# Kernel optimization log

Measured on AMD Instinct MI355X. Metric: run time of the kernel, lower is better.

## Reference

```python
import jax, jax.numpy as jnp
import numpy as np

B, L = 2048, 64          # sentence pairs, leaves per balanced binary tree
V, IN, M, HID, NC = 50000, 300, 150, 50, 5


def setup_inputs() -> dict:
    key = jax.random.key(0)
    ks = jax.random.split(key, 16)
    lin = lambda k, fi, fo: jax.random.normal(k, (fi, fo), jnp.float32) / np.sqrt(fi).astype(np.float32)
    bias = lambda k, fo: jax.random.normal(k, (fo,), jnp.float32) * 0.01
    return {
        "ltokens": jax.random.randint(ks[0], (B, L), 0, V, dtype=jnp.int32),
        "rtokens": jax.random.randint(ks[1], (B, L), 0, V, dtype=jnp.int32),
        "emb":   jax.random.normal(ks[2], (V, IN), jnp.float32),
        "Wioux": lin(ks[3], IN, 3 * M), "bioux": bias(ks[4], 3 * M),
        "Wiouh": lin(ks[5], M, 3 * M), "biouh": bias(ks[6], 3 * M),
        "Wfx":   lin(ks[7], IN, M),    "bfx":   bias(ks[8], M),
        "Wfh":   lin(ks[9], M, M),     "bfh":   bias(ks[10], M),
        "Wh":    lin(ks[11], 2 * M, HID), "bh": bias(ks[12], HID),
        "Wp":    lin(ks[13], HID, NC),    "bp": bias(ks[14], NC),
    }


def _split_iou(iou, m):
    return iou[..., :m], iou[..., m:2 * m], iou[..., 2 * m:]


def _encode(tokens, emb, Wioux, bioux, Wiouh, biouh, Wfh, bfh):
    m = Wfh.shape[0]
    x = emb[tokens]                                   # [B, L, IN]
    # Leaves: child_h = child_c = 0, so iouh contributes only its bias and fc = 0.
    iou = x @ Wioux + bioux + biouh                   # [B, L, 3M]
    i, o, u = _split_iou(iou, m)
    c = jax.nn.sigmoid(i) * jnp.tanh(u)
    h = jax.nn.sigmoid(o) * jnp.tanh(c)
    # Internal nodes level by level (inputs=None branch of node_forward).
    while h.shape[1] > 1:
        Bq, n, _ = h.shape
        ch = h.reshape(Bq, n // 2, 2, m)              # children h
        cc = c.reshape(Bq, n // 2, 2, m)              # children c
        iou = ch.sum(axis=2) @ Wiouh + biouh          # child-sum
        i, o, u = _split_iou(iou, m)
        f = jax.nn.sigmoid(ch @ Wfh + bfh)            # per-child forget gate
        c = jax.nn.sigmoid(i) * jnp.tanh(u) + (f * cc).sum(axis=2)
        h = jax.nn.sigmoid(o) * jnp.tanh(c)
    # ROOT in the original just passes its single child's state through.
    return h[:, 0]                                    # [B, M]


def reference(ltokens, rtokens, emb, Wioux, bioux, Wiouh, biouh, Wfx, bfx, Wfh, bfh, Wh, bh, Wp, bp):
    lh = _encode(ltokens, emb, Wioux, bioux, Wiouh, biouh, Wfh, bfh)
    rh = _encode(rtokens, emb, Wioux, bioux, Wiouh, biouh, Wfh, bfh)
    vec = jnp.concatenate([lh * rh, jnp.abs(lh - rh)], axis=-1)   # [B, 2M]
    mid = jax.nn.sigmoid(vec @ Wh + bh)
    return jax.nn.log_softmax(mid @ Wp + bp, axis=-1)             # [B, NC]
```

## Files before the change

### kernel.cpp

```cpp
#include <hip/hip_runtime.h>
#include <hip/hip_bf16.h>
#include <math.h>

constexpr int B_   = 2048;
constexpr int L_   = 64;
constexpr int V_   = 50000;
constexpr int IN_  = 300;
constexpr int M_   = 150;
constexpr int HID_ = 50;
constexpr int NC_  = 5;

constexpr int KP_  = 160;
constexpr int CS_  = 152;
constexpr int GN_  = 608;
constexpr int GNT_ = 19;
constexpr int GKC_ = 5;
constexpr int GCH_ = GN_ * 32;
constexpr int GQS_ = GN_ * 8;
constexpr int LEAF_N  = 480;
constexpr int LEAF_NT = 15;
constexpr int LEAF_KC = 10;
constexpr int LEAF_CH = LEAF_N * 32;
constexpr int LEAF_QS = LEAF_N * 8;

typedef float f32x4  __attribute__((ext_vector_type(4)));
typedef short bf16x8 __attribute__((ext_vector_type(8)));
typedef short short4v __attribute__((ext_vector_type(4)));

__device__ __forceinline__ float rcp_f(float x) { return __builtin_amdgcn_rcpf(x); }
__device__ __forceinline__ float sgm(float x)   { return rcp_f(1.0f + __expf(-x)); }
__device__ __forceinline__ float tanh_f(float x){ return 1.0f - 2.0f * rcp_f(1.0f + __expf(2.0f * x)); }

__device__ __forceinline__ short f2bs(float f) {
    union { __hip_bfloat16 h; short s; } u; u.h = __float2bfloat16(f); return u.s;
}
__device__ __forceinline__ float bs2f(short s) {
    union { short s; __hip_bfloat16 h; } u; u.s = s; return __bfloat162float(u.h);
}

__device__ __forceinline__ void gl_lds16(const short* g, short* l) {
    __builtin_amdgcn_global_load_lds(
        (const __attribute__((address_space(1))) unsigned int*)g,
        (__attribute__((address_space(3))) unsigned int*)l, 16, 0, 0);
}

__global__ __launch_bounds__(256) void prep_kernel(
    const float* __restrict__ Wioux, const float* __restrict__ Wiouh,
    const float* __restrict__ Wfh, short* __restrict__ Bg, short* __restrict__ Bx)
{
    const int tid = blockIdx.x * blockDim.x + threadIdx.x;
    const int nthr = gridDim.x * blockDim.x;
    const int tot1 = GKC_ * GCH_;
    for (int idx = tid; idx < tot1; idx += nthr) {
        const int kc = idx / GCH_;
        int rem = idx % GCH_;
        const int q = rem / GQS_; rem %= GQS_;
        const int n = rem / 8, j = rem % 8;
        const int k = kc * 32 + q * 8 + j;
        const int m = n >> 2, g = n & 3;
        float v = 0.0f;
        if (k < M_ && m < M_)
            v = (g < 3) ? Wiouh[k * 450 + g * 150 + m] : Wfh[k * M_ + m];
        Bg[idx] = f2bs(v);
    }
    const int tot2 = LEAF_KC * LEAF_CH;
    for (int idx = tid; idx < tot2; idx += nthr) {
        const int kc = idx / LEAF_CH;
        int rem = idx % LEAF_CH;
        const int q = rem / LEAF_QS; rem %= LEAF_QS;
        const int n = rem / 8, j = rem % 8;
        const int k = kc * 32 + q * 8 + j;
        float v = (k < IN_ && n < 450) ? Wioux[k * 450 + n] : 0.0f;
        Bx[idx] = f2bs(v);
    }
}

__global__ __launch_bounds__(512) void leafE_gemm(
    const float* __restrict__ emb, const short* __restrict__ Bx,
    const short* __restrict__ Bg,
    const float* __restrict__ bioux, const float* __restrict__ biouh,
    const float* __restrict__ bfh, short* __restrict__ LeafE)
{
    __shared__ __align__(16) char smem[81248];
    short* Bs     = (short*)smem;
    short* AsF    = (short*)(smem + 38912);
    short* As     = AsF;
    short* CinS   = (short*)(smem + 59392);
    float* bias_s = (float*)(smem + 78848);
    float* Es     = (float*)smem;
    short* Os     = Bs;

    const int t = threadIdx.x;
    const int v0 = blockIdx.x * 64;
    const int w = t >> 6, lane = t & 63;
    const int mt = w & 3;
    const int lr = lane & 15, quad = lane >> 4;

    if (t < 600) bias_s[t] = (t < 450) ? (bioux[t] + biouh[t]) : bfh[t - 450];

    const int nt1 = (w >> 2) * LEAF_NT;
    f32x4 acc[GNT_];
    #pragma unroll
    for (int i = 0; i < LEAF_NT; i++) { acc[i][0] = 0; acc[i][1] = 0; acc[i][2] = 0; acc[i][3] = 0; }

    const int arow = t >> 3, apart = t & 7;
    const int av = v0 + arow;
    const int aq = apart >> 1, aj = (apart & 1) * 4;

    for (int kc = 0; kc < LEAF_KC; kc++) {
        const short* bsrc = Bx + (size_t)kc * LEAF_CH;
        #pragma unroll
        for (int i = 0; i < 3; i++)
            gl_lds16(bsrc + (i * 512 + t) * 8, Bs + (i * 512 + (t & ~63)) * 8);
        if (t < 384)
            gl_lds16(bsrc + (1536 + t) * 8, Bs + (1536 + (t & ~63)) * 8);
        {
            const int k0 = kc * 32 + apart * 4;
            float4 x = make_float4(0.f, 0.f, 0.f, 0.f);
            if (av < V_ && k0 < IN_) x = *(const float4*)&emb[(size_t)av * IN_ + k0];
            short4v s;
            s[0] = f2bs(x.x); s[1] = f2bs(x.y); s[2] = f2bs(x.z); s[3] = f2bs(x.w);
            *(short4v*)&As[aq * 512 + arow * 8 + aj] = s;
        }
        __syncthreads();
        bf16x8 a = *(const bf16x8*)&As[quad * 512 + (mt * 16 + lr) * 8];
        #pragma unroll
        for (int i = 0; i < LEAF_NT; i++) {
            bf16x8 b = *(const bf16x8*)&Bs[quad * LEAF_QS + ((nt1 + i) * 16 + lr) * 8];
            acc[i] = __builtin_amdgcn_mfma_f32_16x16x32_bf16(a, b, acc[i], 0, 0, 0);
        }
        __syncthreads();
    }

    for (int mc = 0; mc < 4; mc++) {
        if (mt == mc) {
            #pragma unroll
            for (int i = 0; i < LEAF_NT; i++) {
                const int col = (nt1 + i) * 16 + lr;
                #pragma unroll
                for (int r = 0; r < 4; r++) Es[(quad * 4 + r) * LEAF_N + col] = acc[i][r];
            }
        }
        __syncthreads();
        for (int p = t; p < 640; p += 512) {
            const int rl = p / 40, Q = p % 40;
            const int m0 = 4 * Q;
            short4v hq = {0, 0, 0, 0}, cq = {0, 0, 0, 0};
            if (Q < 38) {
                #pragma unroll
                for (int jj = 0; jj < 4; jj++) {
                    const int m = m0 + jj;
                    if (m < M_) {
                        const float i_ = Es[rl * LEAF_N + m]       + bias_s[m];
                        const float o_ = Es[rl * LEAF_N + m + 150] + bias_s[m + 150];
                        const float u_ = Es[rl * LEAF_N + m + 300] + bias_s[m + 300];
                        const float c = sgm(i_) * tanh_f(u_);
                        const float h = sgm(o_) * tanh_f(c);
                        hq[jj] = f2bs(h); cq[jj] = f2bs(c);
                    }
                }
            }
            const int row = mc * 16 + rl;
            const int kc = m0 >> 5, q = (m0 >> 3) & 3, j0 = m0 & 7;
            *(short4v*)&AsF[(kc * 4 + q) * 512 + row * 8 + j0] = hq;
            if (m0 < M_) *(short4v*)&CinS[row * CS_ + m0] = cq;
        }
        __syncthreads();
    }

    const int nt2 = (w >> 2) * GNT_;
    #pragma unroll
    for (int i = 0; i < GNT_; i++) { acc[i][0] = 0; acc[i][1] = 0; acc[i][2] = 0; acc[i][3] = 0; }

    for (int kc = 0; kc < GKC_; kc++) {
        const short* bsrc = Bg + (size_t)kc * GCH_;
        #pragma unroll
        for (int i = 0; i < 4; i++)
            gl_lds16(bsrc + (i * 512 + t) * 8, Bs + (i * 512 + (t & ~63)) * 8);
        if (t < 384)
            gl_lds16(bsrc + (2048 + t) * 8, Bs + (2048 + (t & ~63)) * 8);
        __syncthreads();
        bf16x8 a = *(const bf16x8*)&AsF[kc * 2048 + quad * 512 + (mt * 16 + lr) * 8];
        #pragma unroll
        for (int i = 0; i < GNT_; i++) {
            bf16x8 b = *(const bf16x8*)&Bs[quad * GQS_ + ((nt2 + i) * 16 + lr) * 8];
            acc[i] = __builtin_amdgcn_mfma_f32_16x16x32_bf16(a, b, acc[i], 0, 0, 0);
        }
        __syncthreads();
    }

    const int c = lane & 15;
    for (int ph = 0; ph < 2; ph++) {
        if ((mt >> 1) == ph) {
            const int rbase = 16 * (mt & 1) + 4 * quad;
            #pragma unroll
            for (int i = 0; i < GNT_; i++) {
                const int col = (nt2 + i) * 16 + c;
                const int m = col >> 2, g = col & 3;
                #pragma unroll
                for (int r = 0; r < 4; r++) {
                    short ov;
                    if (g == 3) {
                        if (m < M_) {
                            const float cc = bs2f(CinS[(32 * ph + rbase + r) * CS_ + m]);
                            ov = f2bs(sgm(acc[i][r] + bias_s[450 + m]) * cc);
                        } else ov = 0;
                    } else ov = f2bs(acc[i][r]);
                    Os[(rbase + r) * GN_ + col] = ov;
                }
            }
        }
        __syncthreads();
        const int vb = v0 + 32 * ph;
        const int4* os4 = (const int4*)Os;
        for (int u = t; u < 2432; u += 512) {
            const int row = u / 76;
            if (vb + row < V_)
                ((int4*)(LeafE + (size_t)(vb + row) * GN_))[u - row * 76] = os4[u];
        }
        __syncthreads();
    }
}

__device__ __forceinline__ void level_epilogue(
    const f32x4* acc, int mt, int nt0, int lane,
    const short* CinS, int cstride, const float* bias_s, short* Hs, short* Cs)
{
    const int q = lane >> 4, c = lane & 15, g = c & 3, lb = lane & ~3;
    #pragma unroll
    for (int i = 0; i < GNT_; i++) {
        const int col = (nt0 + i) * 16 + c;
        const int m = col >> 2;
        const float vA = acc[i][0] + acc[i][1];
        const float vB = acc[i][2] + acc[i][3];
        const float iA = __shfl(vA, lb), oA = __shfl(vA, lb + 1), uA = __shfl(vA, lb + 2);
        const float iB = __shfl(vB, lb), oB = __shfl(vB, lb + 1), uB = __shfl(vB, lb + 2);
        const float fA0 = __shfl(acc[i][0], lb + 3), fA1 = __shfl(acc[i][1], lb + 3);
        const float fB0 = __shfl(acc[i][2], lb + 3), fB1 = __shfl(acc[i][3], lb + 3);
        if (g < 2 && m < M_) {
            const float iv = g ? iB : iA, ov = g ? oB : oA, uv = g ? uB : uA;
            const float fl = g ? fB0 : fA0, fr = g ? fB1 : fA1;
            const int node = 8 * mt + 2 * q + g;
            const int ch = 16 * mt + 4 * q + 2 * g;
            const float cl = bs2f(CinS[ch * cstride + m]);
            const float cr = bs2f(CinS[(ch + 1) * cstride + m]);
            const float bf = bias_s[450 + m];
            const float cv = sgm(iv + bias_s[m]) * tanh_f(uv + bias_s[m + 300])
                           + sgm(fl + bf) * cl + sgm(fr + bf) * cr;
            const float hv = sgm(ov + bias_s[m + 150]) * tanh_f(cv);
            Hs[node * KP_ + m] = f2bs(hv);
            Cs[node * KP_ + m] = f2bs(cv);
        }
    }
}

__global__ __launch_bounds__(512) void level1_fused(
    const int* __restrict__ ltok, const int* __restrict__ rtok,
    const short* __restrict__ LeafE, const short* __restrict__ Bg,
    const float* __restrict__ biouh, const float* __restrict__ bfh,
    short* __restrict__ Hout, short* __restrict__ Cout)
{
    __shared__ __align__(16) char smem[81248];
    short* Bs     = (short*)smem;
    short* AsF    = (short*)(smem + 38912);
    short* CinS   = (short*)(smem + 59392);
    float* bias_s = (float*)(smem + 78848);
    short* Hs = Bs;
    short* Cs = Bs + 32 * KP_;

    const int t = threadIdx.x;
    const int out0 = blockIdx.x * 32;
    const int w = t >> 6, lane = t & 63;
    const int mt = w & 3, nt0 = (w >> 2) * GNT_;
    const int lr = lane & 15, quad = lane >> 4;

    {
        const short* bsrc = Bg;
        #pragma unroll
        for (int i = 0; i < 4; i++)
            gl_lds16(bsrc + (i * 512 + t) * 8, Bs + (i * 512 + (t & ~63)) * 8);
        if (t < 384)
            gl_lds16(bsrc + (2048 + t) * 8, Bs + (2048 + (t & ~63)) * 8);
    }
    if (t < 600) bias_s[t] = (t < 450) ? biouh[t] : bfh[t - 450];
    __syncthreads();

    {
        const int row = t >> 3, qs = t & 7;
        const int half = B_ * L_;
        const int gidx = blockIdx.x * 128 + 2 * row;
        const int tl = (gidx < half) ? ltok[gidx] : rtok[gidx - half];
        const int tr = (gidx + 1 < half) ? ltok[gidx + 1] : rtok[gidx + 1 - half];
        const short* el = LeafE + (size_t)tl * GN_;
        const short* er = LeafE + (size_t)tr * GN_;
        #pragma unroll
        for (int s = 0; s < 5; s++) {
            const int Q = qs + 8 * s;
            short4v hq = {0, 0, 0, 0}, cq = {0, 0, 0, 0};
            if (Q < 38) {
                union { int4 v[2]; short s16[16]; } ue, ur;
                ue.v[0] = *(const int4*)(el + Q * 16);
                ue.v[1] = *(const int4*)(el + Q * 16 + 8);
                ur.v[0] = *(const int4*)(er + Q * 16);
                ur.v[1] = *(const int4*)(er + Q * 16 + 8);
                #pragma unroll
                for (int jj = 0; jj < 4; jj++) {
                    const int m = 4 * Q + jj;
                    if (m < M_) {
                        const float i_ = bs2f(ue.s16[4 * jj])     + bs2f(ur.s16[4 * jj])     + bias_s[m];
                        const float o_ = bs2f(ue.s16[4 * jj + 1]) + bs2f(ur.s16[4 * jj + 1]) + bias_s[m + 150];
                        const float u_ = bs2f(ue.s16[4 * jj + 2]) + bs2f(ur.s16[4 * jj + 2]) + bias_s[m + 300];
                        const float fc = bs2f(ue.s16[4 * jj + 3]) + bs2f(ur.s16[4 * jj + 3]);
                        const float cv = sgm(i_) * tanh_f(u_) + fc;
                        const float hv = sgm(o_) * tanh_f(cv);
                        hq[jj] = f2bs(hv); cq[jj] = f2bs(cv);
                    }
                }
            }
            const int m0 = 4 * Q;
            const int kc = m0 >> 5, q = (m0 >> 3) & 3, j0 = m0 & 7;
            *(short4v*)&AsF[(kc * 4 + q) * 512 + row * 8 + j0] = hq;
            if (m0 < M_) *(short4v*)&CinS[row * CS_ + m0] = cq;
        }
    }

    f32x4 acc[GNT_];
    #pragma unroll
    for (int i = 0; i < GNT_; i++) { acc[i][0] = 0; acc[i][1] = 0; acc[i][2] = 0; acc[i][3] = 0; }

    for (int kc = 0; kc < GKC_; kc++) {
        if (kc > 0) {
            const short* bsrc = Bg + (size_t)kc * GCH_;
            #pragma unroll
            for (int i = 0; i < 4; i++)
                gl_lds16(bsrc + (i * 512 + t) * 8, Bs + (i * 512 + (t & ~63)) * 8);
            if (t < 384)
                gl_lds16(bsrc + (2048 + t) * 8, Bs + (2048 + (t & ~63)) * 8);
        }
        __syncthreads();
        bf16x8 a = *(const bf16x8*)&AsF[kc * 2048 + quad * 512 + (mt * 16 + lr) * 8];
        #pragma unroll
        for (int i = 0; i < GNT_; i++) {
            bf16x8 b = *(const bf16x8*)&Bs[quad * GQS_ + ((nt0 + i) * 16 + lr) * 8];
            acc[i] = __builtin_amdgcn_mfma_f32_16x16x32_bf16(a, b, acc[i], 0, 0, 0);
        }
        __syncthreads();
    }

    if (t < 320) { const int node = t / 10, mm = 150 + t % 10;
                   Hs[node * KP_ + mm] = 0; Cs[node * KP_ + mm] = 0; }
    level_epilogue(acc, mt, nt0, lane, CinS, CS_, bias_s, Hs, Cs);
    __syncthreads();
    int4* Hg = (int4*)(Hout + (size_t)out0 * KP_);
    int4* Cg = (int4*)(Cout + (size_t)out0 * KP_);
    const int4* hs4 = (const int4*)Hs;
    const int4* cs4 = (const int4*)Cs;
    for (int u = t; u < 1280; u += 512) {
        if (u < 640) Hg[u] = hs4[u]; else Cg[u - 640] = cs4[u - 640];
    }
}

__global__ __launch_bounds__(512) void level_gemm(
    const short* __restrict__ Hin, const short* __restrict__ Cin,
    const short* __restrict__ Bg,
    const float* __restrict__ biouh, const float* __restrict__ bfh,
    short* __restrict__ Hout, short* __restrict__ Cout)
{
    __shared__ __align__(16) char smem[GCH_ * 2 + 4096 + 20480 + 2400];
    short* Bs     = (short*)smem;
    short* As     = (short*)(smem + GCH_ * 2);
    short* CinS   = (short*)(smem + GCH_ * 2 + 4096);
    float* bias_s = (float*)(smem + GCH_ * 2 + 4096 + 20480);
    short* Hs = Bs;
    short* Cs = Bs + 32 * KP_;

    const int t = threadIdx.x;
    const int row0 = blockIdx.x * 64, out0 = blockIdx.x * 32;
    const int w = t >> 6, lane = t & 63;
    const int mt = w & 3, nt0 = (w >> 2) * GNT_;
    const int lr = lane & 15, quad = lane >> 4;

    if (t < 600) bias_s[t] = (t < 450) ? biouh[t] : bfh[t - 450];
    const short* csrc = Cin + (size_t)row0 * KP_;
    #pragma unroll
    for (int i = 0; i < 2; i++)
        gl_lds16(csrc + (i * 512 + t) * 8, CinS + (i * 512 + (t & ~63)) * 8);
    if (t < 256)
        gl_lds16(csrc + (1024 + t) * 8, CinS + (1024 + (t & ~63)) * 8);

    f32x4 acc[GNT_];
    #pragma unroll
    for (int i = 0; i < GNT_; i++) { acc[i][0] = 0; acc[i][1] = 0; acc[i][2] = 0; acc[i][3] = 0; }

    const short* asrc = Hin + (size_t)(row0 + (t & 63)) * KP_ + (t >> 6) * 8;

    for (int kc = 0; kc < GKC_; kc++) {
        const short* bsrc = Bg + (size_t)kc * GCH_;
        #pragma unroll
        for (int i = 0; i < 4; i++)
            gl_lds16(bsrc + (i * 512 + t) * 8, Bs + (i * 512 + (t & ~63)) * 8);
        if (t < 384)
            gl_lds16(bsrc + (2048 + t) * 8, Bs + (2048 + (t & ~63)) * 8);
        if (t < 256)
            gl_lds16(asrc + kc * 32, As + (t & ~63) * 8);
        __syncthreads();
        bf16x8 a = *(const bf16x8*)&As[quad * 512 + (mt * 16 + lr) * 8];
        #pragma unroll
        for (int i = 0; i < GNT_; i++) {
            bf16x8 b = *(const bf16x8*)&Bs[quad * GQS_ + ((nt0 + i) * 16 + lr) * 8];
            acc[i] = __builtin_amdgcn_mfma_f32_16x16x32_bf16(a, b, acc[i], 0, 0, 0);
        }
        __syncthreads();
    }

    if (t < 320) { const int node = t / 10, mm = 150 + t % 10;
                   Hs[node * KP_ + mm] = 0; Cs[node * KP_ + mm] = 0; }
    level_epilogue(acc, mt, nt0, lane, CinS, KP_, bias_s, Hs, Cs);
    __syncthreads();
    int4* Hg = (int4*)(Hout + (size_t)out0 * KP_);
    int4* Cg = (int4*)(Cout + (size_t)out0 * KP_);
    const int4* hs4 = (const int4*)Hs;
    const int4* cs4 = (const int4*)Cs;
    for (int u = t; u < 1280; u += 512) {
        if (u < 640) Hg[u] = hs4[u]; else Cg[u - 640] = cs4[u - 640];
    }
}

__global__ __launch_bounds__(64) void head_kernel(
    const short* __restrict__ RootH,
    const float* __restrict__ Wh, const float* __restrict__ bh,
    const float* __restrict__ Wp, const float* __restrict__ bp,
    float* __restrict__ out)
{
    __shared__ float vec[2 * M_];
    __shared__ float mid[HID_];
    __shared__ float lg[NC_];
    __shared__ float lse;

    const int b = blockIdx.x;
    const int t = threadIdx.x;
    const short* lh = RootH + (size_t)b * KP_;
    const short* rh = RootH + (size_t)(B_ + b) * KP_;

    for (int i = t; i < M_; i += 64) {
        const float a = bs2f(lh[i]), c = bs2f(rh[i]);
        vec[i]      = a * c;
        vec[M_ + i] = fabsf(a - c);
    }
    __syncthreads();

    for (int j = t; j < HID_; j += 64) {
        float acc = bh[j];
        for (int k = 0; k < 2 * M_; k++) acc += vec[k] * Wh[k * HID_ + j];
        mid[j] = sgm(acc);
    }
    __syncthreads();

    if (t < NC_) {
        float acc = bp[t];
        for (int k = 0; k < HID_; k++) acc += mid[k] * Wp[k * NC_ + t];
        lg[t] = acc;
    }
    __syncthreads();

    if (t == 0) {
        float mx = lg[0];
        for (int i = 1; i < NC_; i++) mx = fmaxf(mx, lg[i]);
        float s = 0.0f;
        for (int i = 0; i < NC_; i++) s += expf(lg[i] - mx);
        lse = mx + logf(s);
    }
    __syncthreads();

    if (t < NC_) out[b * NC_ + t] = lg[t] - lse;
}

extern "C" void kernel_launch(void* const* d_in, const int* in_sizes, int n_in,
                              void* d_out, int out_size, void* d_ws, size_t ws_size,
                              hipStream_t stream)
{
    const int*   ltok  = (const int*)d_in[0];
    const int*   rtok  = (const int*)d_in[1];
    const float* emb   = (const float*)d_in[2];
    const float* Wioux = (const float*)d_in[3];
    const float* bioux = (const float*)d_in[4];
    const float* Wiouh = (const float*)d_in[5];
    const float* biouh = (const float*)d_in[6];
    const float* Wfh   = (const float*)d_in[9];
    const float* bfh   = (const float*)d_in[10];
    const float* Wh    = (const float*)d_in[11];
    const float* bh    = (const float*)d_in[12];
    const float* Wp    = (const float*)d_in[13];
    const float* bp    = (const float*)d_in[14];
    float* out = (float*)d_out;

    char* ws = (char*)d_ws;
    size_t off = 0;
    auto carve = [&](size_t bytes) { char* p = ws + off; off += (bytes + 255) & ~(size_t)255; return p; };
    short* Bg    = (short*)carve((size_t)GKC_ * GCH_ * 2);
    short* Bx    = (short*)carve((size_t)LEAF_KC * LEAF_CH * 2);
    short* LeafE = (short*)carve((size_t)V_ * GN_ * 2);
    short* HA    = (short*)carve((size_t)65536 * KP_ * 2);
    short* CA    = (short*)carve((size_t)65536 * KP_ * 2);
    short* HB    = (short*)carve((size_t)32768 * KP_ * 2);
    short* CB    = (short*)carve((size_t)32768 * KP_ * 2);

    hipLaunchKernelGGL(prep_kernel, dim3(128), dim3(256), 0, stream, Wioux, Wiouh, Wfh, Bg, Bx);
    hipLaunchKernelGGL(leafE_gemm, dim3((V_ + 63) / 64), dim3(512), 0, stream,
                       emb, Bx, Bg, bioux, biouh, bfh, LeafE);
    hipLaunchKernelGGL(level1_fused, dim3(2048), dim3(512), 0, stream,
                       ltok, rtok, LeafE, Bg, biouh, bfh, HA, CA);
    hipLaunchKernelGGL(level_gemm, dim3(1024), dim3(512), 0, stream,
                       HA, CA, Bg, biouh, bfh, HB, CB);
    hipLaunchKernelGGL(level_gemm, dim3(512), dim3(512), 0, stream,
                       HB, CB, Bg, biouh, bfh, HA, CA);
    hipLaunchKernelGGL(level_gemm, dim3(256), dim3(512), 0, stream,
                       HA, CA, Bg, biouh, bfh, HB, CB);
    hipLaunchKernelGGL(level_gemm, dim3(128), dim3(512), 0, stream,
                       HB, CB, Bg, biouh, bfh, HA, CA);
    hipLaunchKernelGGL(head_kernel, dim3(B_), dim3(64), 0, stream, HA, Wh, bh, Wp, bp, out);
}
```

Baseline: 543.8 us.

## Double level-kernel tile to 128 rows, keep A fragments in registers, store directly

The level kernels now use 1024-thread blocks covering 128 child rows (64 parents), so each B weight chunk loaded into LDS is reused by twice as many MFMA rows. The A operand (child h) is loaded once into per-lane bf16x8 registers for all K chunks instead of being staged through LDS each iteration. The epilogue writes h and c straight to global memory instead of staging them in LDS. The trade-off is fewer blocks on the late levels, which lowers parallelism, plus higher register pressure and uncoalesced scattered bf16 stores.

```diff
diff --git a/kernel.cpp b/kernel.cpp
--- a/kernel.cpp
+++ b/kernel.cpp
@@ -222,9 +222,10 @@
     }
 }
 
-__device__ __forceinline__ void level_epilogue(
-    const f32x4* acc, int mt, int nt0, int lane,
-    const short* CinS, int cstride, const float* bias_s, short* Hs, short* Cs)
+__device__ __forceinline__ void epilogue128(
+    const f32x4* acc, int mt, int nt0, int lane, int out0,
+    const short* CinS, const float* bias_s,
+    short* __restrict__ Hout, short* __restrict__ Cout)
 {
     const int q = lane >> 4, c = lane & 15, g = c & 3, lb = lane & ~3;
     #pragma unroll
@@ -242,86 +243,86 @@
             const float fl = g ? fB0 : fA0, fr = g ? fB1 : fA1;
             const int node = 8 * mt + 2 * q + g;
             const int ch = 16 * mt + 4 * q + 2 * g;
-            const float cl = bs2f(CinS[ch * cstride + m]);
-            const float cr = bs2f(CinS[(ch + 1) * cstride + m]);
+            const float cl = bs2f(CinS[ch * CS_ + m]);
+            const float cr = bs2f(CinS[(ch + 1) * CS_ + m]);
             const float bf = bias_s[450 + m];
             const float cv = sgm(iv + bias_s[m]) * tanh_f(uv + bias_s[m + 300])
                            + sgm(fl + bf) * cl + sgm(fr + bf) * cr;
             const float hv = sgm(ov + bias_s[m + 150]) * tanh_f(cv);
-            Hs[node * KP_ + m] = f2bs(hv);
-            Cs[node * KP_ + m] = f2bs(cv);
-        }
-    }
-}
-
-__global__ __launch_bounds__(512) void level1_fused(
+            Hout[(size_t)(out0 + node) * KP_ + m] = f2bs(hv);
+            Cout[(size_t)(out0 + node) * KP_ + m] = f2bs(cv);
+        }
+    }
+}
+
+__global__ __launch_bounds__(1024) void level1_fused(
     const int* __restrict__ ltok, const int* __restrict__ rtok,
     const short* __restrict__ LeafE, const short* __restrict__ Bg,
     const float* __restrict__ biouh, const float* __restrict__ bfh,
     short* __restrict__ Hout, short* __restrict__ Cout)
 {
-    __shared__ __align__(16) char smem[81248];
+    __shared__ __align__(16) char smem[80224];
     short* Bs     = (short*)smem;
-    short* AsF    = (short*)(smem + 38912);
-    short* CinS   = (short*)(smem + 59392);
-    float* bias_s = (float*)(smem + 78848);
-    short* Hs = Bs;
-    short* Cs = Bs + 32 * KP_;
+    short* CinS   = (short*)(smem + 38912);
+    float* bias_s = (float*)(smem + 77824);
 
     const int t = threadIdx.x;
-    const int out0 = blockIdx.x * 32;
+    const int out0 = blockIdx.x * 64;
     const int w = t >> 6, lane = t & 63;
-    const int mt = w & 3, nt0 = (w >> 2) * GNT_;
+    const int mt = w & 7, nt0 = (w >> 3) * GNT_;
     const int lr = lane & 15, quad = lane >> 4;
 
     {
-        const short* bsrc = Bg;
-        #pragma unroll
-        for (int i = 0; i < 4; i++)
-            gl_lds16(bsrc + (i * 512 + t) * 8, Bs + (i * 512 + (t & ~63)) * 8);
+        #pragma unroll
+        for (int i = 0; i < 2; i++)
+            gl_lds16(Bg + (i * 1024 + t) * 8, Bs + (i * 1024 + (t & ~63)) * 8);
         if (t < 384)
-            gl_lds16(bsrc + (2048 + t) * 8, Bs + (2048 + (t & ~63)) * 8);
+            gl_lds16(Bg + (2048 + t) * 8, Bs + (2048 + (t & ~63)) * 8);
     }
     if (t < 600) bias_s[t] = (t < 450) ? biouh[t] : bfh[t - 450];
     __syncthreads();
 
-    {
-        const int row = t >> 3, qs = t & 7;
-        const int half = B_ * L_;
-        const int gidx = blockIdx.x * 128 + 2 * row;
-        const int tl = (gidx < half) ? ltok[gidx] : rtok[gidx - half];
-        const int tr = (gidx + 1 < half) ? ltok[gidx + 1] : rtok[gidx + 1 - half];
-        const short* el = LeafE + (size_t)tl * GN_;
-        const short* er = LeafE + (size_t)tr * GN_;
-        #pragma unroll
-        for (int s = 0; s < 5; s++) {
-            const int Q = qs + 8 * s;
-            short4v hq = {0, 0, 0, 0}, cq = {0, 0, 0, 0};
-            if (Q < 38) {
-                union { int4 v[2]; short s16[16]; } ue, ur;
-                ue.v[0] = *(const int4*)(el + Q * 16);
-                ue.v[1] = *(const int4*)(el + Q * 16 + 8);
-                ur.v[0] = *(const int4*)(er + Q * 16);
-                ur.v[1] = *(const int4*)(er + Q * 16 + 8);
-                #pragma unroll
-                for (int jj = 0; jj < 4; jj++) {
-                    const int m = 4 * Q + jj;
-                    if (m < M_) {
-                        const float i_ = bs2f(ue.s16[4 * jj])     + bs2f(ur.s16[4 * jj])     + bias_s[m];
-                        const float o_ = bs2f(ue.s16[4 * jj + 1]) + bs2f(ur.s16[4 * jj + 1]) + bias_s[m + 150];
-                        const float u_ = bs2f(ue.s16[4 * jj + 2]) + bs2f(ur.s16[4 * jj + 2]) + bias_s[m + 300];
-                        const float fc = bs2f(ue.s16[4 * jj + 3]) + bs2f(ur.s16[4 * jj + 3]);
-                        const float cv = sgm(i_) * tanh_f(u_) + fc;
-                        const float hv = sgm(o_) * tanh_f(cv);
-                        hq[jj] = f2bs(hv); cq[jj] = f2bs(cv);
-                    }
+    const int ar = mt * 16 + lr;
+    const int gidx = blockIdx.x * 256 + 2 * ar;
+    const int half = B_ * L_;
+    const int tl = (gidx < half) ? ltok[gidx] : rtok[gidx - half];
+    const int tr = (gidx + 1 < half) ? ltok[gidx + 1] : rtok[gidx + 1 - half];
+    const short* el = LeafE + (size_t)tl * GN_;
+    const short* er = LeafE + (size_t)tr * GN_;
+
+    bf16x8 aF[GKC_];
+    #pragma unroll
+    for (int kc = 0; kc < GKC_; kc++) {
+        const int m0 = kc * 32 + quad * 8;
+        union { bf16x8 v; short s[8]; } hq; union { int4 v; short s[8]; } cq4;
+        #pragma unroll
+        for (int jj = 0; jj < 8; jj++) { hq.s[jj] = 0; cq4.s[jj] = 0; }
+        if (m0 < M_) {
+            union { int4 v[4]; short s[32]; } ue, ur;
+            const short* ep = el + kc * 128 + quad * 32;
+            const short* rp = er + kc * 128 + quad * 32;
+            #pragma unroll
+            for (int j = 0; j < 4; j++) {
+                ue.v[j] = ((const int4*)ep)[j];
+                ur.v[j] = ((const int4*)rp)[j];
+            }
+            #pragma unroll
+            for (int jj = 0; jj < 8; jj++) {
+                const int m = m0 + jj;
+                if (m < M_) {
+                    const float i_ = bs2f(ue.s[4 * jj])     + bs2f(ur.s[4 * jj])     + bias_s[m];
+                    const float o_ = bs2f(ue.s[4 * jj + 1]) + bs2f(ur.s[4 * jj + 1]) + bias_s[m + 150];
+                    const float u_ = bs2f(ue.s[4 * jj + 2]) + bs2f(ur.s[4 * jj + 2]) + bias_s[m + 300];
+                    const float fc = bs2f(ue.s[4 * jj + 3]) + bs2f(ur.s[4 * jj + 3]);
+                    const float cv = sgm(i_) * tanh_f(u_) + fc;
+                    const float hv = sgm(o_) * tanh_f(cv);
+                    hq.s[jj] = f2bs(hv); cq4.s[jj] = f2bs(cv);
                 }
             }
-            const int m0 = 4 * Q;
-            const int kc = m0 >> 5, q = (m0 >> 3) & 3, j0 = m0 & 7;
-            *(short4v*)&AsF[(kc * 4 + q) * 512 + row * 8 + j0] = hq;
-            if (m0 < M_) *(short4v*)&CinS[row * CS_ + m0] = cq;
-        }
+            if (w < 8)
+                *(int4*)&CinS[ar * CS_ + m0] = cq4.v;
+        }
+        aF[kc] = hq.v;
     }
 
     f32x4 acc[GNT_];
@@ -332,97 +333,94 @@
         if (kc > 0) {
             const short* bsrc = Bg + (size_t)kc * GCH_;
             #pragma unroll
-            for (int i = 0; i < 4; i++)
-                gl_lds16(bsrc + (i * 512 + t) * 8, Bs + (i * 512 + (t & ~63)) * 8);
+            for (int i = 0; i < 2; i++)
+                gl_lds16(bsrc + (i * 1024 + t) * 8, Bs + (i * 1024 + (t & ~63)) * 8);
             if (t < 384)
                 gl_lds16(bsrc + (2048 + t) * 8, Bs + (2048 + (t & ~63)) * 8);
         }
         __syncthreads();
-        bf16x8 a = *(const bf16x8*)&AsF[kc * 2048 + quad * 512 + (mt * 16 + lr) * 8];
         #pragma unroll
         for (int i = 0; i < GNT_; i++) {
             bf16x8 b = *(const bf16x8*)&Bs[quad * GQS_ + ((nt0 + i) * 16 + lr) * 8];
-            acc[i] = __builtin_amdgcn_mfma_f32_16x16x32_bf16(a, b, acc[i], 0, 0, 0);
-        }
-        __syncthreads();
-    }
-
-    if (t < 320) { const int node = t / 10, mm = 150 + t % 10;
-                   Hs[node * KP_ + mm] = 0; Cs[node * KP_ + mm] = 0; }
-    level_epilogue(acc, mt, nt0, lane, CinS, CS_, bias_s, Hs, Cs);
-    __syncthreads();
-    int4* Hg = (int4*)(Hout + (size_t)out0 * KP_);
-    int4* Cg = (int4*)(Cout + (size_t)out0 * KP_);
-    const int4* hs4 = (const int4*)Hs;
-    const int4* cs4 = (const int4*)Cs;
-    for (int u = t; u < 1280; u += 512) {
-        if (u < 640) Hg[u] = hs4[u]; else Cg[u - 640] = cs4[u - 640];
-    }
-}
-
-__global__ __launch_bounds__(512) void level_gemm(
+            acc[i] = __builtin_amdgcn_mfma_f32_16x16x32_bf16(aF[kc], b, acc[i], 0, 0, 0);
+        }
+        __syncthreads();
+    }
+
+    epilogue128(acc, mt, nt0, lane, out0, CinS, bias_s, Hout, Cout);
+    if (t < 640) {
+        const int node = t / 10, mm = 150 + t % 10;
+        Hout[(size_t)(out0 + node) * KP_ + mm] = 0;
+        Cout[(size_t)(out0 + node) * KP_ + mm] = 0;
+    }
+}
+
+__global__ __launch_bounds__(1024) void level_gemm(
     const short* __restrict__ Hin, const short* __restrict__ Cin,
     const short* __restrict__ Bg,
     const float* __restrict__ biouh, const float* __restrict__ bfh,
     short* __restrict__ Hout, short* __restrict__ Cout)
 {
-    __shared__ __align__(16) char smem[GCH_ * 2 + 4096 + 20480 + 2400];
+    __shared__ __align__(16) char smem[80224];
     short* Bs     = (short*)smem;
-    short* As     = (short*)(smem + GCH_ * 2);
-    short* CinS   = (short*)(smem + GCH_ * 2 + 4096);
-    float* bias_s = (float*)(smem + GCH_ * 2 + 4096 + 20480);
-    short* Hs = Bs;
-    short* Cs = Bs + 32 * KP_;
+    short* CinS   = (short*)(smem + 38912);
+    float* bias_s = (float*)(smem + 77824);
 
     const int t = threadIdx.x;
-    const int row0 = blockIdx.x * 64, out0 = blockIdx.x * 32;
+    const int row0 = blockIdx.x * 128, out0 = blockIdx.x * 64;
     const int w = t >> 6, lane = t & 63;
-    const int mt = w & 3, nt0 = (w >> 2) * GNT_;
+    const int mt = w & 7, nt0 = (w >> 3) * GNT_;
     const int lr = lane & 15, quad = lane >> 4;
 
     if (t < 600) bias_s[t] = (t < 450) ? biouh[t] : bfh[t - 450];
-    const short* csrc = Cin + (size_t)row0 * KP_;
-    #pragma unroll
-    for (int i = 0; i < 2; i++)
-        gl_lds16(csrc + (i * 512 + t) * 8, CinS + (i * 512 + (t & ~63)) * 8);
-    if (t < 256)
-        gl_lds16(csrc + (1024 + t) * 8, CinS + (1024 + (t & ~63)) * 8);
+
+    {
+        const short* cbase = Cin + (size_t)row0 * KP_;
+        #pragma unroll
+        for (int i = 0; i < 2; i++) {
+            const int u = i * 1024 + t;
+            gl_lds16(cbase + (size_t)(u / 19) * KP_ + (u % 19) * 8,
+                     CinS + (i * 1024 + (t & ~63)) * 8);
+        }
+        if (t < 384) {
+            const int u = 2048 + t;
+            gl_lds16(cbase + (size_t)(u / 19) * KP_ + (u % 19) * 8,
+                     CinS + (2048 + (t & ~63)) * 8);
+        }
+    }
+
+    bf16x8 aF[GKC_];
+    {
+        const short* ap = Hin + (size_t)(row0 + mt * 16 + lr) * KP_ + quad * 8;
+        #pragma unroll
+        for (int kc = 0; kc < GKC_; kc++) aF[kc] = *(const bf16x8*)(ap + kc * 32);
+    }
 
     f32x4 acc[GNT_];
     #pragma unroll
     for (int i = 0; i < GNT_; i++) { acc[i][0] = 0; acc[i][1] = 0; acc[i][2] = 0; acc[i][3] = 0; }
 
-    const short* asrc = Hin + (size_t)(row0 + (t & 63)) * KP_ + (t >> 6) * 8;
-
     for (int kc = 0; kc < GKC_; kc++) {
         const short* bsrc = Bg + (size_t)kc * GCH_;
         #pragma unroll
-        for (int i = 0; i < 4; i++)
-            gl_lds16(bsrc + (i * 512 + t) * 8, Bs + (i * 512 + (t & ~63)) * 8);
+        for (int i = 0; i < 2; i++)
+            gl_lds16(bsrc + (i * 1024 + t) * 8, Bs + (i * 1024 + (t & ~63)) * 8);
         if (t < 384)
             gl_lds16(bsrc + (2048 + t) * 8, Bs + (2048 + (t & ~63)) * 8);
-        if (t < 256)
-            gl_lds16(asrc + kc * 32, As + (t & ~63) * 8);
-        __syncthreads();
-        bf16x8 a = *(const bf16x8*)&As[quad * 512 + (mt * 16 + lr) * 8];
+        __syncthreads();
         #pragma unroll
         for (int i = 0; i < GNT_; i++) {
             bf16x8 b = *(const bf16x8*)&Bs[quad * GQS_ + ((nt0 + i) * 16 + lr) * 8];
-            acc[i] = __builtin_amdgcn_mfma_f32_16x16x32_bf16(a, b, acc[i], 0, 0, 0);
-        }
-        __syncthreads();
-    }
-
-    if (t < 320) { const int node = t / 10, mm = 150 + t % 10;
-                   Hs[node * KP_ + mm] = 0; Cs[node * KP_ + mm] = 0; }
-    level_epilogue(acc, mt, nt0, lane, CinS, KP_, bias_s, Hs, Cs);
-    __syncthreads();
-    int4* Hg = (int4*)(Hout + (size_t)out0 * KP_);
-    int4* Cg = (int4*)(Cout + (size_t)out0 * KP_);
-    const int4* hs4 = (const int4*)Hs;
-    const int4* cs4 = (const int4*)Cs;
-    for (int u = t; u < 1280; u += 512) {
-        if (u < 640) Hg[u] = hs4[u]; else Cg[u - 640] = cs4[u - 640];
+            acc[i] = __builtin_amdgcn_mfma_f32_16x16x32_bf16(aF[kc], b, acc[i], 0, 0, 0);
+        }
+        __syncthreads();
+    }
+
+    epilogue128(acc, mt, nt0, lane, out0, CinS, bias_s, Hout, Cout);
+    if (t < 640) {
+        const int node = t / 10, mm = 150 + t % 10;
+        Hout[(size_t)(out0 + node) * KP_ + mm] = 0;
+        Cout[(size_t)(out0 + node) * KP_ + mm] = 0;
     }
 }
 
@@ -499,24 +497,24 @@
     auto carve = [&](size_t bytes) { char* p = ws + off; off += (bytes + 255) & ~(size_t)255; return p; };
     short* Bg    = (short*)carve((size_t)GKC_ * GCH_ * 2);
     short* Bx    = (short*)carve((size_t)LEAF_KC * LEAF_CH * 2);
-    short* LeafE = (short*)carve((size_t)V_ * GN_ * 2);
+    short* LeafE = (short*)carve((size_t)(V_ + 64) * GN_ * 2);
     short* HA    = (short*)carve((size_t)65536 * KP_ * 2);
     short* CA    = (short*)carve((size_t)65536 * KP_ * 2);
     short* HB    = (short*)carve((size_t)32768 * KP_ * 2);
     short* CB    = (short*)carve((size_t)32768 * KP_ * 2);
 
-    hipLaunchKernelGGL(prep_kernel, dim3(128), dim3(256), 0, stream, Wioux, Wiouh, Wfh, Bg, Bx);
+    hipLaunchKernelGGL(prep_kernel, dim3(256), dim3(256), 0, stream, Wioux, Wiouh, Wfh, Bg, Bx);
     hipLaunchKernelGGL(leafE_gemm, dim3((V_ + 63) / 64), dim3(512), 0, stream,
                        emb, Bx, Bg, bioux, biouh, bfh, LeafE);
-    hipLaunchKernelGGL(level1_fused, dim3(2048), dim3(512), 0, stream,
+    hipLaunchKernelGGL(level1_fused, dim3(1024), dim3(1024), 0, stream,
                        ltok, rtok, LeafE, Bg, biouh, bfh, HA, CA);
-    hipLaunchKernelGGL(level_gemm, dim3(1024), dim3(512), 0, stream,
+    hipLaunchKernelGGL(level_gemm, dim3(512), dim3(1024), 0, stream,
                        HA, CA, Bg, biouh, bfh, HB, CB);
-    hipLaunchKernelGGL(level_gemm, dim3(512), dim3(512), 0, stream,
+    hipLaunchKernelGGL(level_gemm, dim3(256), dim3(1024), 0, stream,
                        HB, CB, Bg, biouh, bfh, HA, CA);
-    hipLaunchKernelGGL(level_gemm, dim3(256), dim3(512), 0, stream,
+    hipLaunchKernelGGL(level_gemm, dim3(128), dim3(1024), 0, stream,
                        HA, CA, Bg, biouh, bfh, HB, CB);
-    hipLaunchKernelGGL(level_gemm, dim3(128), dim3(512), 0, stream,
+    hipLaunchKernelGGL(level_gemm, dim3(64), dim3(1024), 0, stream,
                        HB, CB, Bg, biouh, bfh, HA, CA);
     hipLaunchKernelGGL(head_kernel, dim3(B_), dim3(64), 0, stream, HA, Wh, bh, Wp, bp, out);
 }
```

Result: slower. 708.7 us (+30.3%).
